# Performance work log

Hardware: AMD Instinct MI355X
Metric: run time of the kernel (lower is better)

The kernel has to match this reference:

```python
import jax, jax.numpy as jnp
import numpy as np

N_NODES = 100000   # B*A = 4 * 25000 nodes after the reshape in forward()
N_EDGES = 1600000  # avg degree 16
F_IN = 2           # node_features
HID = 64           # hidden_size
K = 3              # diffusion order (hardcoded in RecurrentGCN)


def _glorot(key, shape):
    fan_in, fan_out = shape[-2], shape[-1]
    s = float(np.sqrt(6.0 / (fan_in + fan_out)))
    return jax.random.uniform(key, shape, jnp.float32, -s, s)


def setup_inputs() -> dict:
    key = jax.random.key(0)
    ks = jax.random.split(key, 12)
    x = jax.random.normal(ks[0], (4, 25000, 12, F_IN), dtype=jnp.float32)
    edge_index = jax.random.randint(ks[1], (2, N_EDGES), 0, N_NODES, dtype=jnp.int32)
    edge_weight = jax.random.uniform(ks[2], (N_EDGES,), dtype=jnp.float32)

    def cell(k, cin):
        kw = jax.random.split(k, 3)
        # 3 gates (z, r, h), each a DConv with weight [2, K, cin, HID]
        W = jnp.stack([_glorot(kw[i], (2, K, cin, HID)) for i in range(3)])
        b = jnp.zeros((3, HID), dtype=jnp.float32)
        return W, b

    enc1_W, enc1_b = cell(ks[3], F_IN + HID)
    enc2_W, enc2_b = cell(ks[4], HID + HID)
    dec1_W, dec1_b = cell(ks[5], F_IN + HID)
    dec2_W, dec2_b = cell(ks[6], HID + HID)
    lin_W = _glorot(ks[7], (HID, F_IN))
    lin_b = jnp.zeros((F_IN,), dtype=jnp.float32)
    return dict(x=x, edge_index=edge_index, edge_weight=edge_weight,
                enc1_W=enc1_W, enc1_b=enc1_b, enc2_W=enc2_W, enc2_b=enc2_b,
                dec1_W=dec1_W, dec1_b=dec1_b, dec2_W=dec2_W, dec2_b=dec2_b,
                lin_W=lin_W, lin_b=lin_b)


def _dconv(v, src, dst, do_inv, di_inv, W, b):
    # Dual-direction diffusion conv (DConv, torch_geometric_temporal), order K.
    # Normalization is applied at the node level before gather so the
    # edge-level multiply (E x C) never needs to be a stored residual.
    def pout(u):  # out[dst] += deg_out_inv[src] * u[src]
        return jax.ops.segment_sum((do_inv[:, None] * u)[src], dst, num_segments=N_NODES)

    def pin(u):   # out[src] += deg_in_inv[dst] * u[dst]
        return jax.ops.segment_sum((di_inv[:, None] * u)[dst], src, num_segments=N_NODES)

    H = v @ (W[0, 0] + W[1, 0])
    t1o, t1i = pout(v), pin(v)
    H = H + t1o @ W[0, 1] + t1i @ W[1, 1]
    t0o = t0i = v
    for k in range(2, K):  # Chebyshev-style recurrence
        t2o = 2.0 * pout(t1o) - t0o
        t2i = 2.0 * pin(t1i) - t0i
        H = H + t2o @ W[0, k] + t2i @ W[1, k]
        t0o, t1o = t1o, t2o
        t0i, t1i = t1i, t2i
    return H + b


def _dcrnn(x, h, src, dst, do_inv, di_inv, W, b):
    # GRU cell whose gates are diffusion convolutions over [x, h].
    xh = jnp.concatenate([x, h], axis=1)
    Z = jax.nn.sigmoid(_dconv(xh, src, dst, do_inv, di_inv, W[0], b[0]))
    R = jax.nn.sigmoid(_dconv(xh, src, dst, do_inv, di_inv, W[1], b[1]))
    Ht = jnp.tanh(_dconv(jnp.concatenate([x, R * h], axis=1),
                         src, dst, do_inv, di_inv, W[2], b[2]))
    return Z * h + (1.0 - Z) * Ht


def _forward(x, edge_index, edge_weight,
             enc1_W, enc1_b, enc2_W, enc2_b,
             dec1_W, dec1_b, dec2_W, dec2_b, lin_W, lin_b):
    B, A, S, Fd = x.shape
    # permute(0,1,3,2) then [..., 0] == x[:, :, 0, :]; flatten to [B*A, F]
    xs = x[:, :, 0, :].reshape(B * A, Fd)
    src, dst = edge_index[0], edge_index[1]
    deg_out = jax.ops.segment_sum(edge_weight, src, num_segments=N_NODES)
    deg_in = jax.ops.segment_sum(edge_weight, dst, num_segments=N_NODES)
    do_inv = jnp.where(deg_out > 0, 1.0 / deg_out, 0.0)
    di_inv = jnp.where(deg_in > 0, 1.0 / deg_in, 0.0)
    zeros = jnp.zeros((B * A, HID), dtype=x.dtype)
    h_enc1 = _dcrnn(xs, zeros, src, dst, do_inv, di_inv, enc1_W, enc1_b)
    h = jax.nn.relu(h_enc1)
    h_enc2 = _dcrnn(h, zeros, src, dst, do_inv, di_inv, enc2_W, enc2_b)
    h = _dcrnn(xs, h_enc1, src, dst, do_inv, di_inv, dec1_W, dec1_b)
    h = jax.nn.relu(h)
    h = _dcrnn(h, h_enc2, src, dst, do_inv, di_inv, dec2_W, dec2_b)
    return h @ lin_W + lin_b


def reference(x, edge_index, edge_weight,
              enc1_W, enc1_b, enc2_W, enc2_b,
              dec1_W, dec1_b, dec2_W, dec2_b, lin_W, lin_b):
    return _forward(x, edge_index, edge_weight,
                    enc1_W, enc1_b, enc2_W, enc2_b,
                    dec1_W, dec1_b, dec2_W, dec2_b, lin_W, lin_b)
```

## Files before the change

### kernel.cpp

```cpp
#include <hip/hip_runtime.h>

#define N_NODES 100000
#define N_EDGES 1600000

typedef _Float16 f16;
typedef _Float16 f16x8 __attribute__((ext_vector_type(8)));
typedef float f32x4 __attribute__((ext_vector_type(4)));

__device__ __forceinline__ float sigf(float x) { return 1.f / (1.f + __expf(-x)); }


__global__ void count_kernel(const int* __restrict__ src, const int* __restrict__ dst,
                             int* __restrict__ cntO, int* __restrict__ cntI,
                             int* __restrict__ slotO, int* __restrict__ slotI)
{
    int i = blockIdx.x * 256 + threadIdx.x;
    if (i >= N_EDGES) return;
    slotO[i] = atomicAdd(&cntO[dst[i]], 1);
    slotI[i] = atomicAdd(&cntI[src[i]], 1);
}

__global__ __launch_bounds__(1024) void scan2_kernel(const int* __restrict__ cntA, int* __restrict__ rpA,
                                                     const int* __restrict__ cntB, int* __restrict__ rpB,
                                                     int n)
{
    const int* cnt = blockIdx.x ? cntB : cntA;
    int* rp = blockIdx.x ? rpB : rpA;
    __shared__ int wsum[16];
    __shared__ int carry;
    int tid = threadIdx.x, lane = tid & 63, wid = tid >> 6;
    if (tid == 0) { rp[0] = 0; carry = 0; }
    __syncthreads();
    for (int base = 0; base < n; base += 1024) {
        int idx = base + tid;
        int x = (idx < n) ? cnt[idx] : 0;
        #pragma unroll
        for (int off = 1; off < 64; off <<= 1) {
            int y = __shfl_up(x, off);
            if (lane >= off) x += y;
        }
        if (lane == 63) wsum[wid] = x;
        __syncthreads();
        if (wid == 0 && lane < 16) {
            int y = wsum[lane];
            #pragma unroll
            for (int off = 1; off < 16; off <<= 1) {
                int z = __shfl_up(y, off);
                if (lane >= off) y += z;
            }
            wsum[lane] = y;
        }
        __syncthreads();
        int tot = x + (wid ? wsum[wid - 1] : 0) + carry;
        if (idx < n) rp[idx + 1] = tot;
        __syncthreads();
        if (tid == 1023) carry = tot;
        __syncthreads();
    }
}

__global__ void fill_kernel(const int* __restrict__ src, const int* __restrict__ dst,
                            const float* __restrict__ ew,
                            const int* __restrict__ rpO, const int* __restrict__ rpI,
                            const int* __restrict__ slotO, const int* __restrict__ slotI,
                            int2* __restrict__ adj2O, int2* __restrict__ adj2I)
{
    int i = blockIdx.x * 256 + threadIdx.x;
    if (i >= N_EDGES) return;
    int s = src[i], d = dst[i];
    int wb = __float_as_int(ew[i]);
    int2 eo; eo.x = s; eo.y = wb;
    adj2O[rpO[d] + slotO[i]] = eo;
    int2 ei; ei.x = d; ei.y = wb;
    adj2I[rpI[s] + slotI[i]] = ei;
}

__global__ void finalize_kernel(const int* __restrict__ rpO, const int2* __restrict__ adj2O,
                                float* __restrict__ di_inv,
                                const int* __restrict__ rpI, const int2* __restrict__ adj2I,
                                float* __restrict__ do_inv)
{
    int n = blockIdx.x * 256 + threadIdx.x;
    if (n >= N_NODES) return;
    float s = 0.f;
    for (int e = rpO[n]; e < rpO[n + 1]; ++e) s += __int_as_float(adj2O[e].y);
    di_inv[n] = (s > 0.f) ? 1.f / s : 0.f;
    float t = 0.f;
    for (int e = rpI[n]; e < rpI[n + 1]; ++e) t += __int_as_float(adj2I[e].y);
    do_inv[n] = (t > 0.f) ? 1.f / t : 0.f;
}

__global__ void coeff_kernel(int2* __restrict__ adj2O, const float* __restrict__ do_inv,
                             int2* __restrict__ adj2I, const float* __restrict__ di_inv)
{
    int i = blockIdx.x * 256 + threadIdx.x;
    if (i >= N_EDGES) return;
    int2 v = adj2O[i]; v.y = __float_as_int(do_inv[v.x]); adj2O[i] = v;
    int2 w = adj2I[i]; w.y = __float_as_int(di_inv[w.x]); adj2I[i] = w;
}

__global__ void prep_w(const float* __restrict__ W, int C, int SA, int PWA, int rA,
                       int gLo, int gHi, int COLS, int XS, f16* __restrict__ outw)
{
    int total = (SA + XS) * COLS * 32;
    int idx = blockIdx.x * 256 + threadIdx.x;
    if (idx >= total) return;
    int k32 = idx & 31;
    int c = (idx >> 5) % COLS;
    int s = (idx >> 5) / COLS;
    int g = (c < 64 || gHi < 0) ? gLo : gHi;
    int col = (c >= 64) ? c - 64 : c;
    int p, r;
    if (s < SA) { p = s / PWA; r = rA + (s % PWA) * 32 + k32; }
    else {
        if (k32 < 10) { p = k32 >> 1; r = k32 & 1; }
        else { outw[idx] = (f16)0.f; return; }
    }
    auto wv = [&](int d, int k) {
        return W[((((size_t)(g * 2 + d) * 3 + k) * C + r) << 6) + col];
    };
    float val;
    if (p == 0)      val = wv(0, 0) + wv(1, 0) - wv(0, 2) - wv(1, 2);
    else if (p == 1) val = wv(0, 1);
    else if (p == 2) val = 2.f * wv(0, 2);
    else if (p == 3) val = wv(1, 1);
    else             val = 2.f * wv(1, 2);
    outw[idx] = (f16)val;
}

__global__ void prep_enc1w(const float* __restrict__ W, float* __restrict__ outw)
{
    int idx = blockIdx.x * 256 + threadIdx.x;
    if (idx >= 1280) return;
    int c = idx & 127, k = idx >> 7;
    int g = (c < 64) ? 0 : 2, col = c & 63;
    int p = k >> 1, r = k & 1;
    const int C = 66;
    auto wv = [&](int d, int kk) {
        return W[((((size_t)(g * 2 + d) * 3 + kk) * C + r) << 6) + col];
    };
    float val;
    if (p == 0)      val = wv(0, 0) + wv(1, 0) - wv(0, 2) - wv(1, 2);
    else if (p == 1) val = wv(0, 1);
    else if (p == 2) val = 2.f * wv(0, 2);
    else if (p == 3) val = wv(1, 1);
    else             val = 2.f * wv(1, 2);
    outw[idx] = val;
}

__global__ void xcat_init(const float* __restrict__ x, f16* __restrict__ xcat)
{
    int i = blockIdx.x * 256 + threadIdx.x;
    if (i >= N_NODES * 32) return;
    int n = i >> 5, c = i & 31;
    float v = (c < 2) ? x[(size_t)n * 24 + c] : 0.f;
    xcat[i] = (f16)v;
}

__global__ void prop2d_kernel(const int* __restrict__ rpA, const int2* __restrict__ adjA,
                              int cinA, int coutA,
                              const int* __restrict__ rpB, const int2* __restrict__ adjB,
                              int cinB, int coutB,
                              f16* __restrict__ xcat)
{
    const int* rp; const int2* adj; int cin, cout;
    if (blockIdx.y == 0) { rp = rpA; adj = adjA; cin = cinA; cout = coutA; }
    else                 { rp = rpB; adj = adjB; cin = cinB; cout = coutB; }
    int n = blockIdx.x * 256 + threadIdx.x;
    if (n >= N_NODES) return;
    int beg = rp[n], end = rp[n + 1];
    float a0 = 0.f, a1 = 0.f;
    for (int e = beg; e < end; ++e) {
        int2 v = adj[e];
        float w = __int_as_float(v.y);
        a0 += w * (float)xcat[((size_t)v.x << 5) + cin];
        a1 += w * (float)xcat[((size_t)v.x << 5) + cin + 1];
    }
    xcat[((size_t)n << 5) + cout] = (f16)a0;
    xcat[((size_t)n << 5) + cout + 1] = (f16)a1;
}

template <int LPN>
__global__ __launch_bounds__(256) void propk(
    const int* __restrict__ rpA, const int2* __restrict__ adjA,
    const f16* __restrict__ uA, f16* __restrict__ oA,
    const int* __restrict__ rpB, const int2* __restrict__ adjB,
    const f16* __restrict__ uB, f16* __restrict__ oB,
    int ldu, int ldo)
{
    const int* RP; const int2* ADJ; const f16* U; f16* OUT;
    if (blockIdx.y == 0) { RP = rpA; ADJ = adjA; U = uA; OUT = oA; }
    else                 { RP = rpB; ADJ = adjB; U = uB; OUT = oB; }
    constexpr int NPB = 256 / LPN;
    int node = blockIdx.x * NPB + (threadIdx.x / LPN);
    int l = threadIdx.x % LPN;
    if (node >= N_NODES) return;
    int b = RP[node], e = RP[node + 1];
    float a[8] = {0.f, 0.f, 0.f, 0.f, 0.f, 0.f, 0.f, 0.f};
    float c[8] = {0.f, 0.f, 0.f, 0.f, 0.f, 0.f, 0.f, 0.f};
    int i = b;
    for (; i + 1 < e; i += 2) {
        int2 n0 = ADJ[i], n1 = ADJ[i + 1];
        float w0 = __int_as_float(n0.y), w1 = __int_as_float(n1.y);
        f16x8 u0 = *(const f16x8*)(U + (size_t)n0.x * ldu + (l << 3));
        f16x8 u1 = *(const f16x8*)(U + (size_t)n1.x * ldu + (l << 3));
        #pragma unroll
        for (int j = 0; j < 8; ++j) { a[j] += w0 * (float)u0[j]; c[j] += w1 * (float)u1[j]; }
    }
    if (i < e) {
        int2 n0 = ADJ[i];
        float w = __int_as_float(n0.y);
        f16x8 u0 = *(const f16x8*)(U + (size_t)n0.x * ldu + (l << 3));
        #pragma unroll
        for (int j = 0; j < 8; ++j) a[j] += w * (float)u0[j];
    }
    f16x8 r;
    #pragma unroll
    for (int j = 0; j < 8; ++j) r[j] = (f16)(a[j] + c[j]);
    *(f16x8*)(OUT + (size_t)node * ldo + (l << 3)) = r;
}

template <int SA, int XS, int COLS, int ACT>
__global__ __launch_bounds__(256) void mfma_gemm(
    const f16* __restrict__ uA, const f16* __restrict__ tA0, const f16* __restrict__ tA1,
    const f16* __restrict__ tA2, const f16* __restrict__ tA3,
    int lAu, int cAu, int lAt, int cAt,
    const f16* __restrict__ xcat, const f16* __restrict__ wstep,
    const f16* __restrict__ addX, int axs,
    const float* __restrict__ biasLo, const float* __restrict__ biasHi,
    f16* __restrict__ out, int os,
    const f16* __restrict__ hmul, int hs,
    f16* __restrict__ out2, int o2s, const f16* __restrict__ zin)
{
    __shared__ f16 As[64][72];
    __shared__ f16 Ws[COLS][72];
    const int row0 = blockIdx.x * 64;
    const int tid = threadIdx.x;
    const int wave = tid >> 6, lane = tid & 63;
    const int lr = lane & 15, lk = lane >> 4;
    const int ka = lk << 3;
    constexpr int RT = (COLS == 128) ? 4 : 2;
    constexpr int PWA = SA / 5;
    constexpr int STEPS = SA + XS;
    constexpr int NIT = (STEPS + 1) / 2;
    f32x4 acc[RT][2] = {};
    const f16* tA[4] = { tA0, tA1, tA2, tA3 };

    #pragma unroll
    for (int sp = 0; sp < NIT; ++sp) {
        const int s0 = sp * 2;
        const int nsub = (s0 + 2 <= STEPS) ? 2 : 1;
        __syncthreads();
        #pragma unroll
        for (int t = 0; t < nsub; ++t) {
            int s = s0 + t;
            {
                int r = tid >> 2, seg = tid & 3;
                int grow = row0 + r;
                const f16* srcp;
                if (s < SA) {
                    int pp = s / PWA, ch = s % PWA;
                    const f16* base = (pp == 0) ? uA : tA[pp - 1];
                    int ld = (pp == 0) ? lAu : lAt;
                    int co = (pp == 0) ? cAu : cAt;
                    srcp = base + (size_t)grow * ld + co + ch * 32 + (seg << 3);
                } else {
                    srcp = xcat + (((size_t)grow) << 5) + (seg << 3);
                }
                int4 v = (grow < N_NODES) ? *(const int4*)srcp : make_int4(0, 0, 0, 0);
                *(int4*)&As[r][t * 32 + (seg << 3)] = v;
            }
            for (int q = tid; q < COLS * 4; q += 256) {
                int cc = q >> 2, sg = q & 3;
                *(int4*)&Ws[cc][t * 32 + (sg << 3)] =
                    *(const int4*)(wstep + (((size_t)(s * COLS + cc)) << 5) + (sg << 3));
            }
        }
        __syncthreads();
        #pragma unroll
        for (int t = 0; t < nsub; ++t) {
            int kb = t * 32 + ka;
            if (COLS == 128) {
                f16x8 b0 = *(const f16x8*)&Ws[wave * 32 + lr][kb];
                f16x8 b1 = *(const f16x8*)&Ws[wave * 32 + 16 + lr][kb];
                #pragma unroll
                for (int rt = 0; rt < RT; ++rt) {
                    f16x8 a = *(const f16x8*)&As[rt * 16 + lr][kb];
                    acc[rt][0] = __builtin_amdgcn_mfma_f32_16x16x32_f16(a, b0, acc[rt][0], 0, 0, 0);
                    acc[rt][1] = __builtin_amdgcn_mfma_f32_16x16x32_f16(a, b1, acc[rt][1], 0, 0, 0);
                }
            } else {
                f16x8 b0 = *(const f16x8*)&Ws[(wave & 1) * 32 + lr][kb];
                f16x8 b1 = *(const f16x8*)&Ws[(wave & 1) * 32 + 16 + lr][kb];
                #pragma unroll
                for (int rt = 0; rt < RT; ++rt) {
                    f16x8 a = *(const f16x8*)&As[(wave >> 1) * 32 + rt * 16 + lr][kb];
                    acc[rt][0] = __builtin_amdgcn_mfma_f32_16x16x32_f16(a, b0, acc[rt][0], 0, 0, 0);
                    acc[rt][1] = __builtin_amdgcn_mfma_f32_16x16x32_f16(a, b1, acc[rt][1], 0, 0, 0);
                }
            }
        }
    }
    if constexpr (ACT == 4) {
        __shared__ float zbuf[64][65];
        float treg[RT][2][4];
        #pragma unroll
        for (int rt = 0; rt < RT; ++rt)
            #pragma unroll
            for (int ct = 0; ct < 2; ++ct) {
                int col = wave * 32 + ct * 16 + lr;
                #pragma unroll
                for (int j = 0; j < 4; ++j) {
                    int r = rt * 16 + lk * 4 + j;
                    float v = acc[rt][ct][j] + ((col < 64) ? biasLo[col] : biasHi[col - 64]);
                    if (col < 64) zbuf[r][col] = sigf(v);
                    else          treg[rt][ct][j] = tanhf(v);
                }
            }
        __syncthreads();
        #pragma unroll
        for (int rt = 0; rt < RT; ++rt)
            #pragma unroll
            for (int ct = 0; ct < 2; ++ct) {
                int col = wave * 32 + ct * 16 + lr;
                if (col < 64) continue;
                #pragma unroll
                for (int j = 0; j < 4; ++j) {
                    int r = rt * 16 + lk * 4 + j;
                    int grow = row0 + r;
                    if (grow >= N_NODES) continue;
                    float h = (1.f - zbuf[r][col - 64]) * treg[rt][ct][j];
                    out[(size_t)grow * os + (col - 64)] = (f16)h;
                }
            }
    } else if constexpr (ACT == 5) {
        #pragma unroll
        for (int rt = 0; rt < RT; ++rt)
            #pragma unroll
            for (int ct = 0; ct < 2; ++ct) {
                int col = wave * 32 + ct * 16 + lr;
                #pragma unroll
                for (int j = 0; j < 4; ++j) {
                    int grow = row0 + rt * 16 + lk * 4 + j;
                    if (grow >= N_NODES) continue;
                    float v = acc[rt][ct][j] + ((col < 64) ? biasLo[col] : biasHi[col - 64]);
                    float sg = sigf(v);
                    if (col < 64)
                        out[(size_t)grow * os + col] = (f16)sg;
                    else
                        out2[(size_t)grow * o2s + (col - 64)] =
                            (f16)(sg * (float)hmul[(size_t)grow * hs + (col - 64)]);
                }
            }
    } else {
        #pragma unroll
        for (int rt = 0; rt < RT; ++rt) {
            int rbase = (COLS == 128) ? rt * 16 : (wave >> 1) * 32 + rt * 16;
            #pragma unroll
            for (int ct = 0; ct < 2; ++ct) {
                int col = ((COLS == 128) ? wave * 32 : (wave & 1) * 32) + ct * 16 + lr;
                #pragma unroll
                for (int j = 0; j < 4; ++j) {
                    int grow = row0 + rbase + lk * 4 + j;
                    if (grow >= N_NODES) continue;
                    float v = acc[rt][ct][j];
                    if (addX)   v += (float)addX[(size_t)grow * axs + col];
                    if (biasLo) v += (col < 64) ? biasLo[col] : biasHi[col - 64];
                    if (ACT == 2) v = tanhf(v);
                    else if (ACT == 6) {
                        float t = tanhf(v);
                        float z = (float)zin[((size_t)grow << 6) + col];
                        float hv = (float)hmul[(size_t)grow * hs + col];
                        v = fmaxf(z * hv + (1.f - z) * t, 0.f);
                    }
                    out[(size_t)grow * os + col] = (f16)v;
                }
            }
        }
    }
}

__global__ __launch_bounds__(256) void enc1_kernel(const f16* __restrict__ xcat,
                                                   const float* __restrict__ We1,
                                                   const float* __restrict__ b,
                                                   f16* __restrict__ c1)
{
    int node = (blockIdx.x << 2) + (threadIdx.x >> 6);
    int lane = threadIdx.x & 63;
    float az = b[lane], at = b[128 + lane];
    #pragma unroll
    for (int k = 0; k < 10; ++k) {
        float xv = (float)xcat[((size_t)node << 5) + k];
        az += xv * We1[k * 128 + lane];
        at += xv * We1[k * 128 + 64 + lane];
    }
    float z = sigf(az), t = tanhf(at);
    float h = (1.f - z) * t;
    size_t o = (size_t)node * 128 + lane;
    c1[o] = (f16)fmaxf(h, 0.f);
    c1[o + 64] = (f16)h;
}

__global__ __launch_bounds__(256) void final_kernel(const f16* __restrict__ zb,
                                                    const f16* __restrict__ gT,
                                                    const f16* __restrict__ h2,
                                                    const float* __restrict__ lW, const float* __restrict__ lb,
                                                    float* __restrict__ out)
{
    int node = (blockIdx.x << 2) + (threadIdx.x >> 6);
    int lane = threadIdx.x & 63;
    float z = (float)zb[((size_t)node << 6) + lane];
    float d = z * (float)h2[(size_t)node * 128 + lane]
            + (1.f - z) * (float)gT[(size_t)node * 128 + lane];
    float s0 = d * lW[lane * 2];
    float s1 = d * lW[lane * 2 + 1];
    #pragma unroll
    for (int off = 32; off > 0; off >>= 1) {
        s0 += __shfl_down(s0, off);
        s1 += __shfl_down(s1, off);
    }
    if (lane == 0) {
        out[node * 2]     = s0 + lb[0];
        out[node * 2 + 1] = s1 + lb[1];
    }
}


extern "C" void kernel_launch(void* const* d_in, const int* in_sizes, int n_in,
                              void* d_out, int out_size, void* d_ws, size_t ws_size,
                              hipStream_t stream)
{
    (void)in_sizes; (void)n_in; (void)out_size;
    const float* x   = (const float*)d_in[0];
    const int*  eidx = (const int*)d_in[1];
    const float* ew  = (const float*)d_in[2];
    const float* e1W = (const float*)d_in[3];
    const float* e1b = (const float*)d_in[4];
    const float* e2W = (const float*)d_in[5];
    const float* e2b = (const float*)d_in[6];
    const float* d1W = (const float*)d_in[7];
    const float* d1b = (const float*)d_in[8];
    const float* d2W = (const float*)d_in[9];
    const float* d2b = (const float*)d_in[10];
    const float* lW  = (const float*)d_in[11];
    const float* lb  = (const float*)d_in[12];
    const int* src = eidx;
    const int* dst = eidx + N_EDGES;
    const int N = N_NODES, E = N_EDGES;

    char* p = (char*)d_ws;
    auto carve = [&](size_t bytes) { char* r = p; p += (bytes + 255) & ~(size_t)255; return r; };
    size_t NC = (size_t)N * 128 * 2;
    int*   cntO  = (int*)carve((size_t)2 * N * 4);
    int*   cntI  = cntO + N;
    int*   rpO   = (int*)carve((size_t)(N + 1) * 4);
    int*   rpI   = (int*)carve((size_t)(N + 1) * 4);
    int*   slotO = (int*)carve((size_t)2 * E * 4);
    int*   slotI = slotO + E;
    int2*  adj2O = (int2*)carve((size_t)E * 8);
    int2*  adj2I = (int2*)carve((size_t)E * 8);
    f16*   ct0   = (f16*)carve(NC);
    f16*   ct1   = (f16*)carve(NC);
    f16*   ct2   = (f16*)carve(NC);
    f16*   ct3   = (f16*)carve(NC);
    float* do_inv = (float*)carve((size_t)N * 4);
    float* di_inv = (float*)carve((size_t)N * 4);
    f16*   xcat = (f16*)carve((size_t)N * 32 * 2);
    f16*   c1   = (f16*)carve(NC);
    f16*   c2   = (f16*)carve(NC);
    f16* wE2   = (f16*)carve((size_t)10 * 128 * 32 * 2);
    f16* wD1zr = (f16*)carve((size_t)11 * 128 * 32 * 2);
    f16* wD1c  = (f16*)carve((size_t)11 * 64 * 32 * 2);
    f16* wD2zr = (f16*)carve((size_t)20 * 128 * 32 * 2);
    f16* wD2cA = (f16*)carve((size_t)10 * 64 * 32 * 2);
    f16* wD2cB = (f16*)carve((size_t)10 * 64 * 32 * 2);
    float* We1 = (float*)carve((size_t)1280 * 4);

    f16* zb = (f16*)slotO;
    f16* g1 = ct1 + 64;
    f16* gT = ct0 + 64;

    size_t needed = (size_t)(p - (char*)d_ws);
    if (needed > ws_size) return;

    const int eg = (E + 255) / 256;
    const int ng = (N + 255) / 256;
    const int GB = 25000;

    hipMemsetAsync(cntO, 0, (size_t)2 * N * 4, stream);
    count_kernel<<<eg, 256, 0, stream>>>(src, dst, cntO, cntI, slotO, slotI);
    scan2_kernel<<<2, 1024, 0, stream>>>(cntO, rpO, cntI, rpI, N);
    fill_kernel<<<eg, 256, 0, stream>>>(src, dst, ew, rpO, rpI, slotO, slotI, adj2O, adj2I);
    finalize_kernel<<<ng, 256, 0, stream>>>(rpO, adj2O, di_inv, rpI, adj2I, do_inv);
    coeff_kernel<<<eg, 256, 0, stream>>>(adj2O, do_inv, adj2I, di_inv);

    auto wprep = [&](const float* W, int C, int SA, int PWA, int rA,
                     int gLo, int gHi, int COLS, int XS, f16* o) {
        int total = (SA + XS) * COLS * 32;
        prep_w<<<(total + 255) / 256, 256, 0, stream>>>(W, C, SA, PWA, rA, gLo, gHi, COLS, XS, o);
    };
    wprep(e2W, 128, 10, 2, 0,  0,  2, 128, 0, wE2);
    wprep(d1W, 66,  10, 2, 2,  0,  1, 128, 1, wD1zr);
    wprep(d1W, 66,  10, 2, 2,  2, -1,  64, 1, wD1c);
    wprep(d2W, 128, 20, 4, 0,  0,  1, 128, 0, wD2zr);
    wprep(d2W, 128, 10, 2, 0,  2, -1,  64, 0, wD2cA);
    wprep(d2W, 128, 10, 2, 64, 2, -1,  64, 0, wD2cB);
    prep_enc1w<<<5, 256, 0, stream>>>(e1W, We1);

    xcat_init<<<(N * 32 + 255) / 256, 256, 0, stream>>>(x, xcat);
    dim3 ng2(ng, 2);
    prop2d_kernel<<<ng2, 256, 0, stream>>>(rpO, adj2O, 0, 2, rpI, adj2I, 0, 6, xcat);
    prop2d_kernel<<<ng2, 256, 0, stream>>>(rpO, adj2O, 2, 4, rpI, adj2I, 6, 8, xcat);

    auto props128 = [&](const f16* u) {
        dim3 pg(N / 16, 2);
        propk<16><<<pg, 256, 0, stream>>>(rpO, adj2O, u, ct0, rpI, adj2I, u, ct2, 128, 128);
        propk<16><<<pg, 256, 0, stream>>>(rpO, adj2O, ct0, ct1, rpI, adj2I, ct2, ct3, 128, 128);
    };
    auto props64 = [&](const f16* u, int ldu) {
        dim3 pg(N / 32, 2);
        propk<8><<<pg, 256, 0, stream>>>(rpO, adj2O, u, ct0, rpI, adj2I, u, ct2, ldu, 128);
        propk<8><<<pg, 256, 0, stream>>>(rpO, adj2O, ct0, ct1, rpI, adj2I, ct2, ct3, 128, 128);
    };
    const int gg = (N + 63) / 64;

    enc1_kernel<<<GB, 256, 0, stream>>>(xcat, We1, e1b, c1);
    props128(c1);
    mfma_gemm<10, 0, 128, 4><<<gg, 256, 0, stream>>>(
        c1, ct0, ct1, ct2, ct3, 128, 0, 128, 0, nullptr, wE2,
        nullptr, 0, e2b, e2b + 128, c2 + 64, 128, nullptr, 0, nullptr, 0, nullptr);
    mfma_gemm<10, 1, 128, 5><<<gg, 256, 0, stream>>>(
        c1, ct0, ct1, ct2, ct3, 128, 64, 128, 64, xcat, wD1zr,
        nullptr, 0, d1b, d1b + 64, zb, 64, c1 + 64, 128, g1, 128, nullptr);
    props64(g1, 128);
    mfma_gemm<10, 1, 64, 6><<<gg, 256, 0, stream>>>(
        g1, ct0, ct1, ct2, ct3, 128, 0, 128, 0, xcat, wD1c,
        nullptr, 0, d1b + 128, d1b + 128, c2, 128, c1 + 64, 128, nullptr, 0, zb);
    props128(c2);
    mfma_gemm<20, 0, 128, 5><<<gg, 256, 0, stream>>>(
        c2, ct0, ct1, ct2, ct3, 128, 0, 128, 0, nullptr, wD2zr,
        nullptr, 0, d2b, d2b + 64, zb, 64, c2 + 64, 128, g1, 128, nullptr);
    mfma_gemm<10, 0, 64, 0><<<gg, 256, 0, stream>>>(
        c2, ct0, ct1, ct2, ct3, 128, 0, 128, 0, nullptr, wD2cA,
        nullptr, 0, nullptr, nullptr, gT, 128, nullptr, 0, nullptr, 0, nullptr);
    props64(g1, 128);
    mfma_gemm<10, 0, 64, 2><<<gg, 256, 0, stream>>>(
        g1, ct0, ct1, ct2, ct3, 128, 0, 128, 0, nullptr, wD2cB,
        gT, 128, d2b + 128, d2b + 128, gT, 128, nullptr, 0, nullptr, 0, nullptr);
    final_kernel<<<GB, 256, 0, stream>>>(zb, gT, c2 + 64, lW, lb, (float*)d_out);
}
```

Baseline: 1.497 ms.

## Merge weight prep launches, drop coeff pass, single-step GEMM K loop

Replaces the seven weight-prep launches with one prep_all kernel that dispatches on block index. Drops coeff_kernel, so the propagation kernels look up the per-node inverse degree from a separate array at gather time instead of reading a precomputed edge coefficient. The MFMA GEMM now loads one 32-wide K step per synchronisation instead of two, with smaller shared tiles. This saves launches and an edge pass, at the cost of an extra dependent gather per edge in every propagation and twice as many barriers in the GEMM.

```diff
diff --git a/kernel.cpp b/kernel.cpp
--- a/kernel.cpp
+++ b/kernel.cpp
@@ -90,20 +90,11 @@
     do_inv[n] = (t > 0.f) ? 1.f / t : 0.f;
 }
 
-__global__ void coeff_kernel(int2* __restrict__ adj2O, const float* __restrict__ do_inv,
-                             int2* __restrict__ adj2I, const float* __restrict__ di_inv)
-{
-    int i = blockIdx.x * 256 + threadIdx.x;
-    if (i >= N_EDGES) return;
-    int2 v = adj2O[i]; v.y = __float_as_int(do_inv[v.x]); adj2O[i] = v;
-    int2 w = adj2I[i]; w.y = __float_as_int(di_inv[w.x]); adj2I[i] = w;
-}
-
-__global__ void prep_w(const float* __restrict__ W, int C, int SA, int PWA, int rA,
-                       int gLo, int gHi, int COLS, int XS, f16* __restrict__ outw)
+__device__ __forceinline__ void prep_w_dev(const float* __restrict__ W, int C, int SA, int PWA,
+                                           int rA, int gLo, int gHi, int COLS, int XS,
+                                           int idx, f16* __restrict__ outw)
 {
     int total = (SA + XS) * COLS * 32;
-    int idx = blockIdx.x * 256 + threadIdx.x;
     if (idx >= total) return;
     int k32 = idx & 31;
     int c = (idx >> 5) % COLS;
@@ -128,9 +119,9 @@
     outw[idx] = (f16)val;
 }
 
-__global__ void prep_enc1w(const float* __restrict__ W, float* __restrict__ outw)
-{
-    int idx = blockIdx.x * 256 + threadIdx.x;
+__device__ __forceinline__ void prep_enc1_dev(const float* __restrict__ W, int idx,
+                                              float* __restrict__ outw)
+{
     if (idx >= 1280) return;
     int c = idx & 127, k = idx >> 7;
     int g = (c < 64) ? 0 : 2, col = c & 63;
@@ -148,6 +139,22 @@
     outw[idx] = val;
 }
 
+__global__ void prep_all(const float* __restrict__ e1W, const float* __restrict__ e2W,
+                         const float* __restrict__ d1W, const float* __restrict__ d2W,
+                         f16* __restrict__ wE2, f16* __restrict__ wD1zr, f16* __restrict__ wD1c,
+                         f16* __restrict__ wD2zr, f16* __restrict__ wD2cA, f16* __restrict__ wD2cB,
+                         float* __restrict__ We1)
+{
+    int b = blockIdx.x, tid = threadIdx.x;
+    if (b < 160)      prep_w_dev(e2W, 128, 10, 2, 0,  0,  2, 128, 0, b * 256 + tid, wE2);
+    else if (b < 336) prep_w_dev(d1W, 66,  10, 2, 2,  0,  1, 128, 1, (b - 160) * 256 + tid, wD1zr);
+    else if (b < 424) prep_w_dev(d1W, 66,  10, 2, 2,  2, -1,  64, 1, (b - 336) * 256 + tid, wD1c);
+    else if (b < 744) prep_w_dev(d2W, 128, 20, 4, 0,  0,  1, 128, 0, (b - 424) * 256 + tid, wD2zr);
+    else if (b < 824) prep_w_dev(d2W, 128, 10, 2, 0,  2, -1,  64, 0, (b - 744) * 256 + tid, wD2cA);
+    else if (b < 904) prep_w_dev(d2W, 128, 10, 2, 64, 2, -1,  64, 0, (b - 824) * 256 + tid, wD2cB);
+    else              prep_enc1_dev(e1W, (b - 904) * 256 + tid, We1);
+}
+
 __global__ void xcat_init(const float* __restrict__ x, f16* __restrict__ xcat)
 {
     int i = blockIdx.x * 256 + threadIdx.x;
@@ -158,21 +165,21 @@
 }
 
 __global__ void prop2d_kernel(const int* __restrict__ rpA, const int2* __restrict__ adjA,
-                              int cinA, int coutA,
+                              const float* __restrict__ scA, int cinA, int coutA,
                               const int* __restrict__ rpB, const int2* __restrict__ adjB,
-                              int cinB, int coutB,
+                              const float* __restrict__ scB, int cinB, int coutB,
                               f16* __restrict__ xcat)
 {
-    const int* rp; const int2* adj; int cin, cout;
-    if (blockIdx.y == 0) { rp = rpA; adj = adjA; cin = cinA; cout = coutA; }
-    else                 { rp = rpB; adj = adjB; cin = cinB; cout = coutB; }
+    const int* rp; const int2* adj; const float* sc; int cin, cout;
+    if (blockIdx.y == 0) { rp = rpA; adj = adjA; sc = scA; cin = cinA; cout = coutA; }
+    else                 { rp = rpB; adj = adjB; sc = scB; cin = cinB; cout = coutB; }
     int n = blockIdx.x * 256 + threadIdx.x;
     if (n >= N_NODES) return;
     int beg = rp[n], end = rp[n + 1];
     float a0 = 0.f, a1 = 0.f;
     for (int e = beg; e < end; ++e) {
         int2 v = adj[e];
-        float w = __int_as_float(v.y);
+        float w = sc[v.x];
         a0 += w * (float)xcat[((size_t)v.x << 5) + cin];
         a1 += w * (float)xcat[((size_t)v.x << 5) + cin + 1];
     }
@@ -182,15 +189,15 @@
 
 template <int LPN>
 __global__ __launch_bounds__(256) void propk(
-    const int* __restrict__ rpA, const int2* __restrict__ adjA,
+    const int* __restrict__ rpA, const int2* __restrict__ adjA, const float* __restrict__ scA,
     const f16* __restrict__ uA, f16* __restrict__ oA,
-    const int* __restrict__ rpB, const int2* __restrict__ adjB,
+    const int* __restrict__ rpB, const int2* __restrict__ adjB, const float* __restrict__ scB,
     const f16* __restrict__ uB, f16* __restrict__ oB,
     int ldu, int ldo)
 {
-    const int* RP; const int2* ADJ; const f16* U; f16* OUT;
-    if (blockIdx.y == 0) { RP = rpA; ADJ = adjA; U = uA; OUT = oA; }
-    else                 { RP = rpB; ADJ = adjB; U = uB; OUT = oB; }
+    const int* RP; const int2* ADJ; const float* SC; const f16* U; f16* OUT;
+    if (blockIdx.y == 0) { RP = rpA; ADJ = adjA; SC = scA; U = uA; OUT = oA; }
+    else                 { RP = rpB; ADJ = adjB; SC = scB; U = uB; OUT = oB; }
     constexpr int NPB = 256 / LPN;
     int node = blockIdx.x * NPB + (threadIdx.x / LPN);
     int l = threadIdx.x % LPN;
@@ -201,7 +208,7 @@
     int i = b;
     for (; i + 1 < e; i += 2) {
         int2 n0 = ADJ[i], n1 = ADJ[i + 1];
-        float w0 = __int_as_float(n0.y), w1 = __int_as_float(n1.y);
+        float w0 = SC[n0.x], w1 = SC[n1.x];
         f16x8 u0 = *(const f16x8*)(U + (size_t)n0.x * ldu + (l << 3));
         f16x8 u1 = *(const f16x8*)(U + (size_t)n1.x * ldu + (l << 3));
         #pragma unroll
@@ -209,7 +216,7 @@
     }
     if (i < e) {
         int2 n0 = ADJ[i];
-        float w = __int_as_float(n0.y);
+        float w = SC[n0.x];
         f16x8 u0 = *(const f16x8*)(U + (size_t)n0.x * ldu + (l << 3));
         #pragma unroll
         for (int j = 0; j < 8; ++j) a[j] += w * (float)u0[j];
@@ -232,8 +239,8 @@
     const f16* __restrict__ hmul, int hs,
     f16* __restrict__ out2, int o2s, const f16* __restrict__ zin)
 {
-    __shared__ f16 As[64][72];
-    __shared__ f16 Ws[COLS][72];
+    __shared__ f16 As[64][40];
+    __shared__ f16 Ws[COLS][40];
     const int row0 = blockIdx.x * 64;
     const int tid = threadIdx.x;
     const int wave = tid >> 6, lane = tid & 63;
@@ -242,62 +249,51 @@
     constexpr int RT = (COLS == 128) ? 4 : 2;
     constexpr int PWA = SA / 5;
     constexpr int STEPS = SA + XS;
-    constexpr int NIT = (STEPS + 1) / 2;
     f32x4 acc[RT][2] = {};
     const f16* tA[4] = { tA0, tA1, tA2, tA3 };
 
     #pragma unroll
-    for (int sp = 0; sp < NIT; ++sp) {
-        const int s0 = sp * 2;
-        const int nsub = (s0 + 2 <= STEPS) ? 2 : 1;
-        __syncthreads();
-        #pragma unroll
-        for (int t = 0; t < nsub; ++t) {
-            int s = s0 + t;
-            {
-                int r = tid >> 2, seg = tid & 3;
-                int grow = row0 + r;
-                const f16* srcp;
-                if (s < SA) {
-                    int pp = s / PWA, ch = s % PWA;
-                    const f16* base = (pp == 0) ? uA : tA[pp - 1];
-                    int ld = (pp == 0) ? lAu : lAt;
-                    int co = (pp == 0) ? cAu : cAt;
-                    srcp = base + (size_t)grow * ld + co + ch * 32 + (seg << 3);
-                } else {
-                    srcp = xcat + (((size_t)grow) << 5) + (seg << 3);
-                }
-                int4 v = (grow < N_NODES) ? *(const int4*)srcp : make_int4(0, 0, 0, 0);
-                *(int4*)&As[r][t * 32 + (seg << 3)] = v;
-            }
-            for (int q = tid; q < COLS * 4; q += 256) {
-                int cc = q >> 2, sg = q & 3;
-                *(int4*)&Ws[cc][t * 32 + (sg << 3)] =
-                    *(const int4*)(wstep + (((size_t)(s * COLS + cc)) << 5) + (sg << 3));
-            }
+    for (int s = 0; s < STEPS; ++s) {
+        __syncthreads();
+        {
+            int r = tid >> 2, seg = tid & 3;
+            int grow = row0 + r;
+            const f16* srcp;
+            if (s < SA) {
+                int pp = s / PWA, ch = s % PWA;
+                const f16* base = (pp == 0) ? uA : tA[pp - 1];
+                int ld = (pp == 0) ? lAu : lAt;
+                int co = (pp == 0) ? cAu : cAt;
+                srcp = base + (size_t)grow * ld + co + ch * 32 + (seg << 3);
+            } else {
+                srcp = xcat + (((size_t)grow) << 5) + (seg << 3);
+            }
+            int4 v = (grow < N_NODES) ? *(const int4*)srcp : make_int4(0, 0, 0, 0);
+            *(int4*)&As[r][seg << 3] = v;
         }
-        __syncthreads();
-        #pragma unroll
-        for (int t = 0; t < nsub; ++t) {
-            int kb = t * 32 + ka;
-            if (COLS == 128) {
-                f16x8 b0 = *(const f16x8*)&Ws[wave * 32 + lr][kb];
-                f16x8 b1 = *(const f16x8*)&Ws[wave * 32 + 16 + lr][kb];
-                #pragma unroll
-                for (int rt = 0; rt < RT; ++rt) {
-                    f16x8 a = *(const f16x8*)&As[rt * 16 + lr][kb];
-                    acc[rt][0] = __builtin_amdgcn_mfma_f32_16x16x32_f16(a, b0, acc[rt][0], 0, 0, 0);
-                    acc[rt][1] = __builtin_amdgcn_mfma_f32_16x16x32_f16(a, b1, acc[rt][1], 0, 0, 0);
-                }
-            } else {
-                f16x8 b0 = *(const f16x8*)&Ws[(wave & 1) * 32 + lr][kb];
-                f16x8 b1 = *(const f16x8*)&Ws[(wave & 1) * 32 + 16 + lr][kb];
-                #pragma unroll
-                for (int rt = 0; rt < RT; ++rt) {
-                    f16x8 a = *(const f16x8*)&As[(wave >> 1) * 32 + rt * 16 + lr][kb];
-                    acc[rt][0] = __builtin_amdgcn_mfma_f32_16x16x32_f16(a, b0, acc[rt][0], 0, 0, 0);
-                    acc[rt][1] = __builtin_amdgcn_mfma_f32_16x16x32_f16(a, b1, acc[rt][1], 0, 0, 0);
-                }
+        for (int q = tid; q < COLS * 4; q += 256) {
+            int cc = q >> 2, sg = q & 3;
+            *(int4*)&Ws[cc][sg << 3] =
+                *(const int4*)(wstep + (((size_t)(s * COLS + cc)) << 5) + (sg << 3));
+        }
+        __syncthreads();
+        if (COLS == 128) {
+            f16x8 b0 = *(const f16x8*)&Ws[wave * 32 + lr][ka];
+            f16x8 b1 = *(const f16x8*)&Ws[wave * 32 + 16 + lr][ka];
+            #pragma unroll
+            for (int rt = 0; rt < RT; ++rt) {
+                f16x8 a = *(const f16x8*)&As[rt * 16 + lr][ka];
+                acc[rt][0] = __builtin_amdgcn_mfma_f32_16x16x32_f16(a, b0, acc[rt][0], 0, 0, 0);
+                acc[rt][1] = __builtin_amdgcn_mfma_f32_16x16x32_f16(a, b1, acc[rt][1], 0, 0, 0);
+            }
+        } else {
+            f16x8 b0 = *(const f16x8*)&Ws[(wave & 1) * 32 + lr][ka];
+            f16x8 b1 = *(const f16x8*)&Ws[(wave & 1) * 32 + 16 + lr][ka];
+            #pragma unroll
+            for (int rt = 0; rt < RT; ++rt) {
+                f16x8 a = *(const f16x8*)&As[(wave >> 1) * 32 + rt * 16 + lr][ka];
+                acc[rt][0] = __builtin_amdgcn_mfma_f32_16x16x32_f16(a, b0, acc[rt][0], 0, 0, 0);
+                acc[rt][1] = __builtin_amdgcn_mfma_f32_16x16x32_f16(a, b1, acc[rt][1], 0, 0, 0);
             }
         }
     }
@@ -492,35 +488,30 @@
     scan2_kernel<<<2, 1024, 0, stream>>>(cntO, rpO, cntI, rpI, N);
     fill_kernel<<<eg, 256, 0, stream>>>(src, dst, ew, rpO, rpI, slotO, slotI, adj2O, adj2I);
     finalize_kernel<<<ng, 256, 0, stream>>>(rpO, adj2O, di_inv, rpI, adj2I, do_inv);
-    coeff_kernel<<<eg, 256, 0, stream>>>(adj2O, do_inv, adj2I, di_inv);
-
-    auto wprep = [&](const float* W, int C, int SA, int PWA, int rA,
-                     int gLo, int gHi, int COLS, int XS, f16* o) {
-        int total = (SA + XS) * COLS * 32;
-        prep_w<<<(total + 255) / 256, 256, 0, stream>>>(W, C, SA, PWA, rA, gLo, gHi, COLS, XS, o);
-    };
-    wprep(e2W, 128, 10, 2, 0,  0,  2, 128, 0, wE2);
-    wprep(d1W, 66,  10, 2, 2,  0,  1, 128, 1, wD1zr);
-    wprep(d1W, 66,  10, 2, 2,  2, -1,  64, 1, wD1c);
-    wprep(d2W, 128, 20, 4, 0,  0,  1, 128, 0, wD2zr);
-    wprep(d2W, 128, 10, 2, 0,  2, -1,  64, 0, wD2cA);
-    wprep(d2W, 128, 10, 2, 64, 2, -1,  64, 0, wD2cB);
-    prep_enc1w<<<5, 256, 0, stream>>>(e1W, We1);
+
+    prep_all<<<909, 256, 0, stream>>>(e1W, e2W, d1W, d2W,
+                                      wE2, wD1zr, wD1c, wD2zr, wD2cA, wD2cB, We1);
 
     xcat_init<<<(N * 32 + 255) / 256, 256, 0, stream>>>(x, xcat);
     dim3 ng2(ng, 2);
-    prop2d_kernel<<<ng2, 256, 0, stream>>>(rpO, adj2O, 0, 2, rpI, adj2I, 0, 6, xcat);
-    prop2d_kernel<<<ng2, 256, 0, stream>>>(rpO, adj2O, 2, 4, rpI, adj2I, 6, 8, xcat);
+    prop2d_kernel<<<ng2, 256, 0, stream>>>(rpO, adj2O, do_inv, 0, 2,
+                                           rpI, adj2I, di_inv, 0, 6, xcat);
+    prop2d_kernel<<<ng2, 256, 0, stream>>>(rpO, adj2O, do_inv, 2, 4,
+                                           rpI, adj2I, di_inv, 6, 8, xcat);
 
     auto props128 = [&](const f16* u) {
         dim3 pg(N / 16, 2);
-        propk<16><<<pg, 256, 0, stream>>>(rpO, adj2O, u, ct0, rpI, adj2I, u, ct2, 128, 128);
-        propk<16><<<pg, 256, 0, stream>>>(rpO, adj2O, ct0, ct1, rpI, adj2I, ct2, ct3, 128, 128);
+        propk<16><<<pg, 256, 0, stream>>>(rpO, adj2O, do_inv, u, ct0,
+                                          rpI, adj2I, di_inv, u, ct2, 128, 128);
+        propk<16><<<pg, 256, 0, stream>>>(rpO, adj2O, do_inv, ct0, ct1,
+                                          rpI, adj2I, di_inv, ct2, ct3, 128, 128);
     };
     auto props64 = [&](const f16* u, int ldu) {
         dim3 pg(N / 32, 2);
-        propk<8><<<pg, 256, 0, stream>>>(rpO, adj2O, u, ct0, rpI, adj2I, u, ct2, ldu, 128);
-        propk<8><<<pg, 256, 0, stream>>>(rpO, adj2O, ct0, ct1, rpI, adj2I, ct2, ct3, 128, 128);
+        propk<8><<<pg, 256, 0, stream>>>(rpO, adj2O, do_inv, u, ct0,
+                                         rpI, adj2I, di_inv, u, ct2, ldu, 128);
+        propk<8><<<pg, 256, 0, stream>>>(rpO, adj2O, do_inv, ct0, ct1,
+                                         rpI, adj2I, di_inv, ct2, ct3, 128, 128);
     };
     const int gg = (N + 63) / 64;
 
```

Result: slower. 1.535 ms (+2.5%).
